# Kernel tuning notes

Hardware: AMD Instinct MI355X
Metric: run time of the kernel (lower is better)

Reference implementation:

```python
import jax, jax.numpy as jnp
import numpy as np

V = 10000   # vocab_size
L = 12      # n_layer
H = 12      # n_head
C = 768     # n_embd
TE = 64     # t_embd
WTE = C - TE
BS = 1024   # block_size
B, T = 4, 1024
D = C // H
EPS = 1e-5


def setup_inputs() -> dict:
    key = jax.random.key(0)
    ks = jax.random.split(key, 12)
    s = 0.02
    def n(k, shape, extra=1.0):
        return jax.random.normal(k, shape, jnp.float32) * (s * extra)
    resid_scale = 1.0 / np.sqrt(2 * L)  # c_proj init std scaling from _init_weights loop
    return {
        'idx': jax.random.randint(ks[0], (B, T), 0, V),
        'ts': jax.random.uniform(ks[1], (B, T), jnp.float32) * 100.0,
        'wte': n(ks[2], (V, WTE)),
        'basis_freq': jnp.asarray(1.0 / 10 ** np.linspace(0, 9, TE), jnp.float32),
        'phase': jnp.zeros((TE,), jnp.float32),
        'wpe': n(ks[3], (BS, C)),
        'ln1_w': jnp.ones((L, C), jnp.float32), 'ln1_b': jnp.zeros((L, C), jnp.float32),
        'qkv_w': n(ks[4], (L, 3 * C, C)), 'qkv_b': jnp.zeros((L, 3 * C), jnp.float32),
        'proj_w': n(ks[5], (L, C, C), resid_scale), 'proj_b': jnp.zeros((L, C), jnp.float32),
        'ln2_w': jnp.ones((L, C), jnp.float32), 'ln2_b': jnp.zeros((L, C), jnp.float32),
        'fc_w': n(ks[6], (L, 4 * C, C)), 'fc_b': jnp.zeros((L, 4 * C), jnp.float32),
        'fc2_w': n(ks[7], (L, C, 4 * C), resid_scale), 'fc2_b': jnp.zeros((L, C), jnp.float32),
        'lnf_w': jnp.ones((C,), jnp.float32), 'lnf_b': jnp.zeros((C,), jnp.float32),
        'lm_w': n(ks[8], (V, C)),
        'tp_w': n(ks[9], (1, C)),
    }


def _ln(x, w, b):
    mu = jnp.mean(x, -1, keepdims=True)
    var = jnp.mean((x - mu) ** 2, -1, keepdims=True)
    return (x - mu) * jax.lax.rsqrt(var + EPS) * w + b


def reference(idx, ts, wte, basis_freq, phase, wpe, ln1_w, ln1_b, qkv_w, qkv_b,
              proj_w, proj_b, ln2_w, ln2_b, fc_w, fc_b, fc2_w, fc2_b,
              lnf_w, lnf_b, lm_w, tp_w):
    Bv, Tv = idx.shape
    tok = wte[idx]                                      # [B,T,C-TE]
    tim = jnp.cos(ts[..., None] * basis_freq + phase)   # TimeEncode -> [B,T,TE]
    x = jnp.concatenate([tok, tim], axis=-1) + wpe[:Tv]
    mask = jnp.tril(jnp.ones((Tv, Tv), bool))
    scale = 1.0 / np.sqrt(D)

    def block(x, p):
        l1w, l1b, qw, qb, pw, pb, l2w, l2b, fw, fb, f2w, f2b = p
        h = _ln(x, l1w, l1b)
        qkv = h @ qw.T + qb                              # [B,T,3C]
        q, k, v = jnp.split(qkv, 3, axis=-1)
        def heads(z):
            return z.reshape(Bv, Tv, H, D).transpose(0, 2, 1, 3)  # [B,H,T,D]
        q, k, v = heads(q), heads(k), heads(v)
        att = jnp.einsum('bhtd,bhsd->bhts', q, k) * scale
        att = jnp.where(mask, att, -jnp.inf)             # causal masked_fill
        att = jax.nn.softmax(att, axis=-1)
        y = jnp.einsum('bhts,bhsd->bhtd', att, v)
        y = y.transpose(0, 2, 1, 3).reshape(Bv, Tv, C)
        x = x + (y @ pw.T + pb)
        h2 = _ln(x, l2w, l2b)
        m = jax.nn.gelu(h2 @ fw.T + fb, approximate=False)  # torch nn.GELU default is exact
        x = x + (m @ f2w.T + f2b)
        return x, None

    x, _ = jax.lax.scan(block, x, (ln1_w, ln1_b, qkv_w, qkv_b, proj_w, proj_b,
                                   ln2_w, ln2_b, fc_w, fc_b, fc2_w, fc2_b))
    x = _ln(x, lnf_w, lnf_b)
    logits = x @ lm_w.T          # [B,T,V]
    tpred = x @ tp_w.T           # [B,T,1]
    return logits, tpred
```

## Files before the change

### kernel.cpp

```cpp
#include <hip/hip_runtime.h>
#include <hip/hip_bf16.h>
#include <math.h>

#define Bb   4
#define Tt   1024
#define Cc   768
#define Hh   12
#define Dd   64
#define Ll   12
#define Vv   10000
#define WTEe 704
#define MTOT 4096

#define QSCALE 0.18033688f

typedef __bf16 bf16x8 __attribute__((ext_vector_type(8)));
typedef float  f32x4  __attribute__((ext_vector_type(4)));
typedef unsigned short u16;

typedef const __attribute__((address_space(1))) void* gptr_t;
typedef __attribute__((address_space(3))) void* lptr_t;

__device__ inline void gload16(const void* g, void* l) {
    __builtin_amdgcn_global_load_lds((gptr_t)g, (lptr_t)l, 16, 0, 0);
}

__device__ inline u16 f2bf(float f) {
    unsigned int u = __float_as_uint(f);
    return (u16)((u + 0x7fffu + ((u >> 16) & 1u)) >> 16);
}
__device__ inline float bf2f(u16 u) { return __uint_as_float(((unsigned)u) << 16); }

__device__ inline float gelu_f(float v) {
    float t = v * (0.797884561f + 0.0356774081f * v * v);
    float e = __expf(2.f * t);
    float th = 1.f - 2.f / (e + 1.f);
    return 0.5f * v * (1.f + th);
}

#if __has_builtin(__builtin_amdgcn_exp2f)
__device__ inline float fast_exp2(float x) { return __builtin_amdgcn_exp2f(x); }
#else
__device__ inline float fast_exp2(float x) { return exp2f(x); }
#endif

#define WAITVM(N)  asm volatile("s_waitcnt vmcnt(" #N ")" ::: "memory")
#define WAITLGKM0() asm volatile("s_waitcnt lgkmcnt(0)" ::: "memory")
#define SCHEDB()   __builtin_amdgcn_sched_barrier(0)
#define SBAR()     __builtin_amdgcn_s_barrier()

__global__ __launch_bounds__(256)
void convert_pack(const float* __restrict__ in, u16* __restrict__ out,
                  int nk8, int K, int rowmod, int scaleLim)
{
    int i = blockIdx.x * 256 + threadIdx.x;
    if (i >= nk8) return;
    int row = (i << 3) / K;
    int col = (i << 3) % K;
    float s = 1.f;
    if (rowmod && (row % rowmod) < scaleLim) s = QSCALE;
    float4 v0 = ((const float4*)in)[2 * i];
    float4 v1 = ((const float4*)in)[2 * i + 1];
    uint4 o;
    o.x = (unsigned)f2bf(v0.x * s) | ((unsigned)f2bf(v0.y * s) << 16);
    o.y = (unsigned)f2bf(v0.z * s) | ((unsigned)f2bf(v0.w * s) << 16);
    o.z = (unsigned)f2bf(v1.x * s) | ((unsigned)f2bf(v1.y * s) << 16);
    o.w = (unsigned)f2bf(v1.z * s) | ((unsigned)f2bf(v1.w * s) << 16);
    int tile = row >> 4, kt = col >> 5;
    int l = (row & 15) | (((col >> 3) & 3) << 4);
    size_t off = (((size_t)tile * (K >> 5) + kt) << 9) + l * 8;
    *(uint4*)(out + off) = o;
}

__global__ __launch_bounds__(256)
void scale_qkvb(const float* __restrict__ in, float* __restrict__ out, int n)
{
    int i = blockIdx.x * 256 + threadIdx.x;
    if (i >= n) return;
    int col = i % (3 * Cc);
    out[i] = in[i] * (col < Cc ? QSCALE : 1.f);
}

__global__ __launch_bounds__(256)
void embed_kernel(const int* __restrict__ idx, const float* __restrict__ ts,
                  const float* __restrict__ wte, const float* __restrict__ freq,
                  const float* __restrict__ ph, const float* __restrict__ wpe,
                  float* __restrict__ x)
{
    const int bt  = blockIdx.x;
    const int t   = bt & (Tt - 1);
    const int tok = idx[bt];
    const float tv = ts[bt];
#pragma unroll
    for (int j = 0; j < 3; ++j) {
        int c = threadIdx.x + (j << 8);
        float val;
        if (c < WTEe) val = wte[(size_t)tok * WTEe + c];
        else {
            int e = c - WTEe;
            val = cosf(tv * freq[e] + ph[e]);
        }
        x[(size_t)bt * Cc + c] = val + wpe[(size_t)t * Cc + c];
    }
}

__global__ __launch_bounds__(256)
void ln_kernel(const float* __restrict__ x, const float* __restrict__ wt,
               const float* __restrict__ bs, u16* __restrict__ out)
{
    const int row = blockIdx.x;
    const int tid = threadIdx.x;
    const float* xr = x + (size_t)row * Cc;
    float v0 = xr[tid], v1 = xr[tid + 256], v2 = xr[tid + 512];
    float s = v0 + v1 + v2;
#pragma unroll
    for (int m = 32; m; m >>= 1) s += __shfl_xor(s, m);
    __shared__ float red[4];
    const int wv = tid >> 6;
    if ((tid & 63) == 0) red[wv] = s;
    __syncthreads();
    float mu = (red[0] + red[1] + red[2] + red[3]) * (1.f / 768.f);
    float d0 = v0 - mu, d1 = v1 - mu, d2 = v2 - mu;
    float s2 = d0 * d0 + d1 * d1 + d2 * d2;
#pragma unroll
    for (int m = 32; m; m >>= 1) s2 += __shfl_xor(s2, m);
    __syncthreads();
    if ((tid & 63) == 0) red[wv] = s2;
    __syncthreads();
    float var = (red[0] + red[1] + red[2] + red[3]) * (1.f / 768.f);
    float rs = rsqrtf(var + 1e-5f);
    u16* orow = out + (size_t)row * Cc;
    orow[tid]       = f2bf(d0 * rs * wt[tid]       + bs[tid]);
    orow[tid + 256] = f2bf(d1 * rs * wt[tid + 256] + bs[tid + 256]);
    orow[tid + 512] = f2bf(d2 * rs * wt[tid + 512] + bs[tid + 512]);
}

__device__ inline void st_out(float* p, size_t o, float v) { p[o] = v; }
__device__ inline void st_out(u16*   p, size_t o, float v) { p[o] = f2bf(v); }

template<int EPI, typename OutT>
__global__ __launch_bounds__(256)
void gemm_bf16(const u16* __restrict__ A, const u16* __restrict__ Wp,
               const float* __restrict__ bias, const float* __restrict__ resid,
               OutT* __restrict__ out, u16* __restrict__ vt, int N, int K)
{
    __shared__ uint4 AF[3][8][64];
    __shared__ uint4 BF[3][8][64];
    const int tid  = threadIdx.x;
    const int lane = tid & 63;
    const int w    = tid >> 6;
    const int wr   = w >> 1, wc = w & 1;
    const int lq   = lane & 15, g = lane >> 4;
    const int m0   = blockIdx.x * 128, n0 = blockIdx.y * 128;
    const int KB   = K >> 5;

    const int arow0 = m0 + (2 * w) * 16 + lq;
    const int arow1 = arow0 + 16;
    const u16* ap0 = A + (size_t)arow0 * K + g * 8;
    const u16* ap1 = A + (size_t)arow1 * K + g * 8;

    int tn0 = (n0 >> 4) + 2 * w, tn1 = tn0 + 1;
    const int tmax = (N >> 4) - 1;
    tn0 = tn0 < tmax ? tn0 : tmax;
    tn1 = tn1 < tmax ? tn1 : tmax;
    const u16* bq0 = Wp + (((size_t)tn0 * KB) << 9) + lane * 8;
    const u16* bq1 = Wp + (((size_t)tn1 * KB) << 9) + lane * 8;

    f32x4 acc[4][4] = {};
    const int nk = KB;

#define GSTAGE(s, sl) do { int kk_ = (s) << 5;                      \
        gload16(ap0 + kk_, &AF[sl][2 * w][lane]);                   \
        gload16(ap1 + kk_, &AF[sl][2 * w + 1][lane]);               \
        gload16(bq0 + ((size_t)(s) << 9), &BF[sl][2 * w][lane]);    \
        gload16(bq1 + ((size_t)(s) << 9), &BF[sl][2 * w + 1][lane]); } while (0)

    GSTAGE(0, 0);
    GSTAGE(1, 1);
    WAITVM(4);
    SCHEDB();
    SBAR();
    SCHEDB();

    int sl = 0;
    for (int t = 0; t < nk; ++t) {
        int sl2 = sl + 2; if (sl2 >= 3) sl2 -= 3;
        if (t + 2 < nk) GSTAGE(t + 2, sl2);

        bf16x8 af[4], bfr[4];
#pragma unroll
        for (int mi = 0; mi < 4; ++mi)
            af[mi] = __builtin_bit_cast(bf16x8, AF[sl][wr * 4 + mi][lane]);
#pragma unroll
        for (int ni = 0; ni < 4; ++ni)
            bfr[ni] = __builtin_bit_cast(bf16x8, BF[sl][wc * 4 + ni][lane]);
        __builtin_amdgcn_s_setprio(1);
#pragma unroll
        for (int mi = 0; mi < 4; ++mi)
#pragma unroll
            for (int ni = 0; ni < 4; ++ni)
                acc[mi][ni] = __builtin_amdgcn_mfma_f32_16x16x32_bf16(
                    af[mi], bfr[ni], acc[mi][ni], 0, 0, 0);
        __builtin_amdgcn_s_setprio(0);

        if (t + 2 < nk) { WAITVM(4); }
        else           { WAITVM(0); }
        SCHEDB();
        SBAR();
        SCHEDB();
        sl = (sl + 1 == 3) ? 0 : sl + 1;
    }
#undef GSTAGE

    if (EPI == 3 && n0 >= 1536) {
#pragma unroll
        for (int mi = 0; mi < 4; ++mi)
#pragma unroll
            for (int ni = 0; ni < 4; ++ni) {
                int col = n0 + wc * 64 + ni * 16 + lq;
                int c2  = col - 1536;
                int hh  = c2 >> 6, dd = c2 & 63;
                int row = m0 + wr * 64 + mi * 16 + g * 4;
                int bb  = row >> 10, tr = row & 1023;
                float bv = bias[col];
                ushort4 o;
                o.x = f2bf(acc[mi][ni][0] + bv);
                o.y = f2bf(acc[mi][ni][1] + bv);
                o.z = f2bf(acc[mi][ni][2] + bv);
                o.w = f2bf(acc[mi][ni][3] + bv);
                *(ushort4*)&vt[(((size_t)bb * Hh + hh) * Dd + dd) * Tt + tr] = o;
            }
        return;
    }

#pragma unroll
    for (int mi = 0; mi < 4; ++mi)
#pragma unroll
        for (int ni = 0; ni < 4; ++ni) {
            int col = n0 + wc * 64 + ni * 16 + lq;
            if (col >= N) continue;
            int row = m0 + wr * 64 + mi * 16 + g * 4;
            float bv = bias ? bias[col] : 0.f;
#pragma unroll
            for (int q = 0; q < 4; ++q) {
                float v = acc[mi][ni][q] + bv;
                size_t o = (size_t)(row + q) * N + col;
                if (EPI == 1) v += resid[o];
                if (EPI == 2) v = gelu_f(v);
                st_out(out, o, v);
            }
        }
}

template<int EPI, typename OutT>
__global__ __launch_bounds__(256)
void gemm_n64(const u16* __restrict__ A, const u16* __restrict__ Wp,
              const float* __restrict__ bias, const float* __restrict__ resid,
              OutT* __restrict__ out, int N, int K)
{
    __shared__ uint4 AF[3][4][64];
    __shared__ uint4 BF[3][8][64];
    const int tid  = threadIdx.x;
    const int lane = tid & 63;
    const int w    = tid >> 6;
    const int wr   = w & 1, wc = w >> 1;
    const int lq   = lane & 15, g = lane >> 4;
    const int m0   = blockIdx.x * 64, n0 = blockIdx.y * 128;
    const int KB   = K >> 5;

    const u16* ap  = A + (size_t)(m0 + w * 16 + lq) * K + g * 8;
    int tn0 = (n0 >> 4) + 2 * w, tn1 = tn0 + 1;
    const int tmax = (N >> 4) - 1;
    tn0 = tn0 < tmax ? tn0 : tmax;
    tn1 = tn1 < tmax ? tn1 : tmax;
    const u16* bq0 = Wp + (((size_t)tn0 * KB) << 9) + lane * 8;
    const u16* bq1 = Wp + (((size_t)tn1 * KB) << 9) + lane * 8;

    f32x4 acc[2][4] = {};
    const int nk = KB;

#define GSTAGE(s, sl) do { int kk_ = (s) << 5;                      \
        gload16(ap  + kk_, &AF[sl][w][lane]);                       \
        gload16(bq0 + ((size_t)(s) << 9), &BF[sl][2 * w][lane]);    \
        gload16(bq1 + ((size_t)(s) << 9), &BF[sl][2 * w + 1][lane]); } while (0)

    GSTAGE(0, 0);
    GSTAGE(1, 1);
    WAITVM(3);
    SCHEDB();
    SBAR();
    SCHEDB();

    int sl = 0;
    for (int t = 0; t < nk; ++t) {
        int sl2 = sl + 2; if (sl2 >= 3) sl2 -= 3;
        if (t + 2 < nk) GSTAGE(t + 2, sl2);

        bf16x8 af[2], bfr[4];
#pragma unroll
        for (int mi = 0; mi < 2; ++mi)
            af[mi] = __builtin_bit_cast(bf16x8, AF[sl][wr * 2 + mi][lane]);
#pragma unroll
        for (int ni = 0; ni < 4; ++ni)
            bfr[ni] = __builtin_bit_cast(bf16x8, BF[sl][wc * 4 + ni][lane]);
        __builtin_amdgcn_s_setprio(1);
#pragma unroll
        for (int mi = 0; mi < 2; ++mi)
#pragma unroll
            for (int ni = 0; ni < 4; ++ni)
                acc[mi][ni] = __builtin_amdgcn_mfma_f32_16x16x32_bf16(
                    af[mi], bfr[ni], acc[mi][ni], 0, 0, 0);
        __builtin_amdgcn_s_setprio(0);

        if (t + 2 < nk) { WAITVM(3); }
        else           { WAITVM(0); }
        SCHEDB();
        SBAR();
        SCHEDB();
        sl = (sl + 1 == 3) ? 0 : sl + 1;
    }
#undef GSTAGE

#pragma unroll
    for (int mi = 0; mi < 2; ++mi)
#pragma unroll
        for (int ni = 0; ni < 4; ++ni) {
            int col = n0 + wc * 64 + ni * 16 + lq;
            if (col >= N) continue;
            int row = m0 + wr * 32 + mi * 16 + g * 4;
            float bv = bias ? bias[col] : 0.f;
#pragma unroll
            for (int q = 0; q < 4; ++q) {
                float v = acc[mi][ni][q] + bv;
                size_t o = (size_t)(row + q) * N + col;
                if (EPI == 1) v += resid[o];
                if (EPI == 2) v = gelu_f(v);
                st_out(out, o, v);
            }
        }
}

template<int EPI, typename OutT>
__global__ __launch_bounds__(512, 2)
void gemm8p(const u16* __restrict__ A, const u16* __restrict__ Wp,
            const float* __restrict__ bias, const float* __restrict__ resid,
            OutT* __restrict__ out, int N, int K)
{
    __shared__ uint4 AF[2][16][2][64];
    __shared__ uint4 BF[2][16][2][64];
    const int tid  = threadIdx.x;
    const int lane = tid & 63;
    const int w    = tid >> 6;
    const int wr   = w >> 2, wc = w & 3;
    const int lq   = lane & 15, g = lane >> 4;
    const int m0   = blockIdx.x * 256, n0 = blockIdx.y * 256;
    const int KB   = K >> 5;

    const int ar0 = m0 + (2 * w) * 16 + lq;
    const u16* aS0 = A + (size_t)ar0 * K + g * 8;
    const u16* aS1 = aS0 + (size_t)16 * K;

    int tn0 = (n0 >> 4) + 2 * w, tn1 = tn0 + 1;
    const int tmax = (N >> 4) - 1;
    tn0 = tn0 < tmax ? tn0 : tmax;
    tn1 = tn1 < tmax ? tn1 : tmax;
    const u16* bq0 = Wp + (((size_t)tn0 * KB) << 9) + lane * 8;
    const u16* bq1 = Wp + (((size_t)tn1 * KB) << 9) + lane * 8;

    f32x4 acc[8][4] = {};
    const int nt = K >> 6;

    gload16(aS0,      &AF[0][2 * w][0][lane]);
    gload16(aS1,      &AF[0][2 * w + 1][0][lane]);
    gload16(bq0,                 &BF[0][2 * w][0][lane]);
    gload16(bq1,                 &BF[0][2 * w + 1][0][lane]);
    gload16(aS0 + 32, &AF[0][2 * w][1][lane]);
    gload16(aS1 + 32, &AF[0][2 * w + 1][1][lane]);
    gload16(bq0 + 512,           &BF[0][2 * w][1][lane]);
    gload16(bq1 + 512,           &BF[0][2 * w + 1][1][lane]);
    WAITVM(0);
    SCHEDB();
    SBAR();

    int buf = 0;
    for (int t = 0; t < nt; ++t) {
        const bool more = (t + 1 < nt);
        const int kn = (t + 1) << 6;
        const size_t bb0 = (size_t)(2 * (t + 1)) << 9;
        bf16x8 a0[4], a1[4], b0[4];

#pragma unroll
        for (int i = 0; i < 4; ++i)
            a0[i] = __builtin_bit_cast(bf16x8, AF[buf][wr * 8 + i][0][lane]);
#pragma unroll
        for (int i = 0; i < 4; ++i)
            b0[i] = __builtin_bit_cast(bf16x8, BF[buf][wc * 4 + i][0][lane]);
        if (more) {
            gload16(aS0 + kn, &AF[buf ^ 1][2 * w][0][lane]);
            gload16(aS1 + kn, &AF[buf ^ 1][2 * w + 1][0][lane]);
        }
        SCHEDB();
        SBAR();
        WAITLGKM0();
        SCHEDB();
        __builtin_amdgcn_s_setprio(1);
#pragma unroll
        for (int mi = 0; mi < 4; ++mi)
#pragma unroll
            for (int ni = 0; ni < 4; ++ni)
                acc[mi][ni] = __builtin_amdgcn_mfma_f32_16x16x32_bf16(
                    a0[mi], b0[ni], acc[mi][ni], 0, 0, 0);
        __builtin_amdgcn_s_setprio(0);
        SBAR();

#pragma unroll
        for (int i = 0; i < 4; ++i)
            a1[i] = __builtin_bit_cast(bf16x8, AF[buf][wr * 8 + 4 + i][0][lane]);
        if (more) {
            gload16(bq0 + bb0, &BF[buf ^ 1][2 * w][0][lane]);
            gload16(bq1 + bb0, &BF[buf ^ 1][2 * w + 1][0][lane]);
        }
        SCHEDB();
        SBAR();
        WAITLGKM0();
        SCHEDB();
        __builtin_amdgcn_s_setprio(1);
#pragma unroll
        for (int mi = 0; mi < 4; ++mi)
#pragma unroll
            for (int ni = 0; ni < 4; ++ni)
                acc[4 + mi][ni] = __builtin_amdgcn_mfma_f32_16x16x32_bf16(
                    a1[mi], b0[ni], acc[4 + mi][ni], 0, 0, 0);
        __builtin_amdgcn_s_setprio(0);
        if (more) { WAITVM(4); } else { WAITVM(0); }
        SCHEDB();
        SBAR();

#pragma unroll
        for (int i = 0; i < 4; ++i)
            a0[i] = __builtin_bit_cast(bf16x8, AF[buf][wr * 8 + i][1][lane]);
#pragma unroll
        for (int i = 0; i < 4; ++i)
            b0[i] = __builtin_bit_cast(bf16x8, BF[buf][wc * 4 + i][1][lane]);
        if (more) {
            gload16(aS0 + kn + 32, &AF[buf ^ 1][2 * w][1][lane]);
            gload16(aS1 + kn + 32, &AF[buf ^ 1][2 * w + 1][1][lane]);
        }
        SCHEDB();
        SBAR();
        WAITLGKM0();
        SCHEDB();
        __builtin_amdgcn_s_setprio(1);
#pragma unroll
        for (int mi = 0; mi < 4; ++mi)
#pragma unroll
            for (int ni = 0; ni < 4; ++ni)
                acc[mi][ni] = __builtin_amdgcn_mfma_f32_16x16x32_bf16(
                    a0[mi], b0[ni], acc[mi][ni], 0, 0, 0);
        __builtin_amdgcn_s_setprio(0);
        SBAR();

#pragma unroll
        for (int i = 0; i < 4; ++i)
            a1[i] = __builtin_bit_cast(bf16x8, AF[buf][wr * 8 + 4 + i][1][lane]);
        if (more) {
            gload16(bq0 + bb0 + 512, &BF[buf ^ 1][2 * w][1][lane]);
            gload16(bq1 + bb0 + 512, &BF[buf ^ 1][2 * w + 1][1][lane]);
        }
        SCHEDB();
        SBAR();
        WAITLGKM0();
        SCHEDB();
        __builtin_amdgcn_s_setprio(1);
#pragma unroll
        for (int mi = 0; mi < 4; ++mi)
#pragma unroll
            for (int ni = 0; ni < 4; ++ni)
                acc[4 + mi][ni] = __builtin_amdgcn_mfma_f32_16x16x32_bf16(
                    a1[mi], b0[ni], acc[4 + mi][ni], 0, 0, 0);
        __builtin_amdgcn_s_setprio(0);
        if (more) { WAITVM(4); } else { WAITVM(0); }
        SCHEDB();
        SBAR();

        buf ^= 1;
    }

#pragma unroll
    for (int mi = 0; mi < 8; ++mi)
#pragma unroll
        for (int ni = 0; ni < 4; ++ni) {
            int col = n0 + wc * 64 + ni * 16 + lq;
            if (col >= N) continue;
            int row = m0 + wr * 128 + mi * 16 + g * 4;
            float bv = bias ? bias[col] : 0.f;
#pragma unroll
            for (int q = 0; q < 4; ++q) {
                float v = acc[mi][ni][q] + bv;
                size_t o = (size_t)(row + q) * N + col;
                if (EPI == 1) v += resid[o];
                if (EPI == 2) v = gelu_f(v);
                st_out(out, o, v);
            }
        }
}

__global__ __launch_bounds__(512)
void attn_mfma(const u16* __restrict__ qkv, const u16* __restrict__ vt,
               u16* __restrict__ y)
{
    __shared__ uint4 KF[2][4][2][64];
    __shared__ uint4 VF[2][4][2][64];

    const int tid  = threadIdx.x;
    const int lane = tid & 63;
    const int w    = tid >> 6;
    const int lq   = lane & 15, g = lane >> 4;
    const int m    = gridDim.x - 1 - blockIdx.x;
    const int bh   = blockIdx.y;
    const int b    = bh / Hh, h = bh % Hh;
    const int wq0  = m * 128 + w * 16;
    const size_t base = (size_t)b * Tt * (3 * Cc);

    const u16* qrow = qkv + base + (size_t)(wq0 + lq) * (3 * Cc) + h * Dd;
    bf16x8 qf0 = __builtin_bit_cast(bf16x8, *(const uint4*)(qrow + g * 8));
    bf16x8 qf1 = __builtin_bit_cast(bf16x8, *(const uint4*)(qrow + 32 + g * 8));

    f32x4 yac[4] = {};
    float lrun = 0.f;

    const int wm = w & 3;
    const u16* kbase = qkv + base + Cc + h * Dd + (size_t)(wm * 16 + lq) * (3 * Cc) + g * 8;
    const u16* vbase = vt + ((size_t)bh * Dd + wm * 16 + lq) * Tt + g * 8;

#define STAGE(c, bi)  do {                                              \
        if (w < 4) {                                                    \
            const u16* kp = kbase + (size_t)(c) * 64 * (3 * Cc);        \
            gload16(kp,      &KF[bi][wm][0][lane]);                     \
            gload16(kp + 32, &KF[bi][wm][1][lane]);                     \
        } else {                                                        \
            const u16* vp = vbase + (c) * 64;                           \
            gload16(vp,      &VF[bi][wm][0][lane]);                     \
            gload16(vp + 32, &VF[bi][wm][1][lane]);                     \
        }                                                               \
    } while (0)

    const int nch = 2 * m + 2;
    STAGE(0, 0);
    WAITVM(0);
    SCHEDB();
    SBAR();

    const int srcb = lq + ((g & 1) << 5);

    int buf = 0;
    for (int c = 0; c < nch; ++c) {
        if (c + 1 < nch) STAGE(c + 1, buf ^ 1);

        f32x4 sc[4] = {};
        __builtin_amdgcn_s_setprio(1);
#pragma unroll
        for (int nt = 0; nt < 4; ++nt) {
            bf16x8 k0 = __builtin_bit_cast(bf16x8, KF[buf][nt][0][lane]);
            bf16x8 k1 = __builtin_bit_cast(bf16x8, KF[buf][nt][1][lane]);
            sc[nt] = __builtin_amdgcn_mfma_f32_16x16x32_bf16(k0, qf0, sc[nt], 0, 0, 0);
            sc[nt] = __builtin_amdgcn_mfma_f32_16x16x32_bf16(k1, qf1, sc[nt], 0, 0, 0);
        }
        __builtin_amdgcn_s_setprio(0);

        const int s0 = c * 64;
        if (s0 + 63 > wq0) {
            const int qg = wq0 + lq;
#pragma unroll
            for (int nt = 0; nt < 4; ++nt) {
                const int kb = s0 + nt * 16 + (g << 2);
#pragma unroll
                for (int j = 0; j < 4; ++j)
                    if (kb + j > qg) sc[nt][j] = -1e30f;
            }
        }

        float ls = 0.f;
#pragma unroll
        for (int nt = 0; nt < 4; ++nt)
#pragma unroll
            for (int j = 0; j < 4; ++j) {
                float p = fast_exp2(sc[nt][j]);
                sc[nt][j] = p;
                ls += p;
            }
        ls += __shfl_xor(ls, 16);
        ls += __shfl_xor(ls, 32);
        lrun += ls;

        unsigned pk[4][2];
#pragma unroll
        for (int nt = 0; nt < 4; ++nt) {
            unsigned u0 = __float_as_uint(sc[nt][0]);
            unsigned u1 = __float_as_uint(sc[nt][1]);
            unsigned u2 = __float_as_uint(sc[nt][2]);
            unsigned u3 = __float_as_uint(sc[nt][3]);
            pk[nt][0] = (u0 >> 16) | (u1 & 0xffff0000u);
            pk[nt][1] = (u2 >> 16) | (u3 & 0xffff0000u);
        }

        unsigned pa0[4], pa1[4];
#pragma unroll
        for (int m2 = 0; m2 < 4; ++m2) {
            int hsel = m2 & 1;
            int src  = srcb + ((m2 >> 1) << 4);
            unsigned lo0 = __shfl(pk[0][hsel], src);
            unsigned hi0 = __shfl(pk[1][hsel], src);
            unsigned lo1 = __shfl(pk[2][hsel], src);
            unsigned hi1 = __shfl(pk[3][hsel], src);
            pa0[m2] = (g >> 1) ? hi0 : lo0;
            pa1[m2] = (g >> 1) ? hi1 : lo1;
        }
        uint4 A0 = make_uint4(pa0[0], pa0[1], pa0[2], pa0[3]);
        uint4 A1 = make_uint4(pa1[0], pa1[1], pa1[2], pa1[3]);
        bf16x8 pA0 = __builtin_bit_cast(bf16x8, A0);
        bf16x8 pA1 = __builtin_bit_cast(bf16x8, A1);

        __builtin_amdgcn_s_setprio(1);
#pragma unroll
        for (int dt = 0; dt < 4; ++dt) {
            bf16x8 vb0 = __builtin_bit_cast(bf16x8, VF[buf][dt][0][lane]);
            bf16x8 vb1 = __builtin_bit_cast(bf16x8, VF[buf][dt][1][lane]);
            yac[dt] = __builtin_amdgcn_mfma_f32_16x16x32_bf16(pA0, vb0, yac[dt], 0, 0, 0);
            yac[dt] = __builtin_amdgcn_mfma_f32_16x16x32_bf16(pA1, vb1, yac[dt], 0, 0, 0);
        }
        __builtin_amdgcn_s_setprio(0);

        if (c + 1 < nch) { WAITVM(0); }
        SCHEDB();
        SBAR();
        buf ^= 1;
    }
#undef STAGE

    f32x4 rl;
#pragma unroll
    for (int j = 0; j < 4; ++j)
        rl[j] = 1.0f / __shfl(lrun, (g << 2) + j);
#pragma unroll
    for (int dt = 0; dt < 4; ++dt)
#pragma unroll
        for (int j = 0; j < 4; ++j)
            y[(size_t)(b * Tt + wq0 + (g << 2) + j) * Cc + h * Dd + dt * 16 + lq]
                = f2bf(yac[dt][j] * rl[j]);
}

__global__ __launch_bounds__(256)
void tpred_kernel(const u16* __restrict__ h, const float* __restrict__ tp,
                  float* __restrict__ out)
{
    const int row  = blockIdx.x * 4 + (threadIdx.x >> 6);
    const int lane = threadIdx.x & 63;
    const u16* hr = h + (size_t)row * Cc;
    float s = 0.f;
#pragma unroll
    for (int j = 0; j < 12; ++j) s += bf2f(hr[lane + (j << 6)]) * tp[lane + (j << 6)];
#pragma unroll
    for (int m = 32; m; m >>= 1) s += __shfl_xor(s, m);
    if (lane == 0) out[row] = s;
}

extern "C" void kernel_launch(void* const* d_in, const int* in_sizes, int n_in,
                              void* d_out, int out_size, void* d_ws, size_t ws_size,
                              hipStream_t stream)
{
    const int*   idx  = (const int*)d_in[0];
    const float* ts   = (const float*)d_in[1];
    const float* wte  = (const float*)d_in[2];
    const float* freq = (const float*)d_in[3];
    const float* ph   = (const float*)d_in[4];
    const float* wpe  = (const float*)d_in[5];
    const float* ln1w = (const float*)d_in[6];
    const float* ln1b = (const float*)d_in[7];
    const float* qkvw = (const float*)d_in[8];
    const float* qkvb = (const float*)d_in[9];
    const float* pw   = (const float*)d_in[10];
    const float* pb   = (const float*)d_in[11];
    const float* ln2w = (const float*)d_in[12];
    const float* ln2b = (const float*)d_in[13];
    const float* fcw  = (const float*)d_in[14];
    const float* fcb  = (const float*)d_in[15];
    const float* f2w  = (const float*)d_in[16];
    const float* f2b  = (const float*)d_in[17];
    const float* lnfw = (const float*)d_in[18];
    const float* lnfb = (const float*)d_in[19];
    const float* lmw  = (const float*)d_in[20];
    const float* tpw  = (const float*)d_in[21];
    float* out = (float*)d_out;

    const int n_qkvw = 3 * Cc * Cc, n_pw = Cc * Cc, n_fcw = 4 * Cc * Cc;

    char* p = (char*)d_ws;
    float* x    = (float*)p;               p += (size_t)MTOT * Cc * 4;
    u16*   qkvB = (u16*)p;                 p += (size_t)MTOT * 3 * Cc * 2;
    u16*   VtB  = (u16*)p;                 p += (size_t)Bb * Hh * Dd * Tt * 2;
    u16*   hB   = (u16*)p;                 p += (size_t)MTOT * Cc * 2;
    u16*   yB   = (u16*)p;                 p += (size_t)MTOT * Cc * 2;
    u16*   mbB  = (u16*)p;                 p += (size_t)MTOT * 4 * Cc * 2;
    u16*   lmwB = (u16*)p;                 p += (size_t)Vv * Cc * 2;
    float* sbias= (float*)p;               p += (size_t)Ll * 3 * Cc * 4;
    char* wbase = p;

    size_t need_big = (size_t)(wbase - (char*)d_ws)
                    + ((size_t)Ll * (n_qkvw + n_pw + 2 * n_fcw)) * 2;
    bool big = ws_size >= need_big;

    u16 *wqA, *wpA, *wfA, *wf2A;
    if (big) {
        wqA  = (u16*)wbase;                wbase += (size_t)Ll * n_qkvw * 2;
        wpA  = (u16*)wbase;                wbase += (size_t)Ll * n_pw * 2;
        wfA  = (u16*)wbase;                wbase += (size_t)Ll * n_fcw * 2;
        wf2A = (u16*)wbase;
    } else {
        wqA  = (u16*)wbase;                wbase += (size_t)n_qkvw * 2;
        wpA  = (u16*)wbase;                wbase += (size_t)n_pw * 2;
        wfA  = (u16*)wbase;                wbase += (size_t)n_fcw * 2;
        wf2A = (u16*)wbase;
    }

    auto pack = [&](const float* src, u16* dst, size_t rows, int K,
                    int rowmod, int scaleLim) {
        int nk8 = (int)(rows * K / 8);
        convert_pack<<<(nk8 + 255) / 256, 256, 0, stream>>>(
            src, dst, nk8, K, rowmod, scaleLim);
    };

    pack(lmw, lmwB, Vv, Cc, 0, 0);
    {
        int nb = Ll * 3 * Cc;
        scale_qkvb<<<(nb + 255) / 256, 256, 0, stream>>>(qkvb, sbias, nb);
    }
    if (big) {
        pack(qkvw, wqA,  (size_t)Ll * 3 * Cc, Cc, 3 * Cc, Cc);
        pack(pw,   wpA,  (size_t)Ll * Cc,     Cc, 0, 0);
        pack(fcw,  wfA,  (size_t)Ll * 4 * Cc, Cc, 0, 0);
        pack(f2w,  wf2A, (size_t)Ll * Cc, 4 * Cc, 0, 0);
    }
    embed_kernel<<<MTOT, 256, 0, stream>>>(idx, ts, wte, freq, ph, wpe, x);

    for (int l = 0; l < Ll; ++l) {
        u16 *wqB, *wpB, *wfB, *wf2B;
        if (big) {
            wqB  = wqA  + (size_t)l * n_qkvw;
            wpB  = wpA  + (size_t)l * n_pw;
            wfB  = wfA  + (size_t)l * n_fcw;
            wf2B = wf2A + (size_t)l * n_fcw;
        } else {
            wqB = wqA; wpB = wpA; wfB = wfA; wf2B = wf2A;
            pack(qkvw + (size_t)l * n_qkvw, wqB, 3 * Cc, Cc, 3 * Cc, Cc);
            pack(pw   + (size_t)l * n_pw,   wpB, Cc,     Cc, 0, 0);
            pack(fcw  + (size_t)l * n_fcw,  wfB, 4 * Cc, Cc, 0, 0);
            pack(f2w  + (size_t)l * n_fcw,  wf2B, Cc, 4 * Cc, 0, 0);
        }

        ln_kernel<<<MTOT, 256, 0, stream>>>(x, ln1w + l * Cc, ln1b + l * Cc, hB);
        gemm_bf16<3, u16><<<dim3(32, 18), 256, 0, stream>>>(
            hB, wqB, sbias + (size_t)l * 3 * Cc, nullptr, qkvB, VtB, 3 * Cc, Cc);
        attn_mfma<<<dim3(Tt / 128, Bb * Hh), 512, 0, stream>>>(qkvB, VtB, yB);
        gemm_n64<1, float><<<dim3(64, 6), 256, 0, stream>>>(
            yB, wpB, pb + (size_t)l * Cc, x, x, Cc, Cc);
        ln_kernel<<<MTOT, 256, 0, stream>>>(x, ln2w + l * Cc, ln2b + l * Cc, hB);
        gemm_bf16<2, u16><<<dim3(32, 24), 256, 0, stream>>>(
            hB, wfB, fcb + (size_t)l * 4 * Cc, nullptr, mbB, nullptr, 4 * Cc, Cc);
        gemm_n64<1, float><<<dim3(64, 6), 256, 0, stream>>>(
            mbB, wf2B, f2b + (size_t)l * Cc, x, x, Cc, 4 * Cc);
    }

    ln_kernel<<<MTOT, 256, 0, stream>>>(x, lnfw, lnfb, hB);
    gemm8p<0, float><<<dim3(16, 40), 512, 0, stream>>>(
        hB, lmwB, nullptr, nullptr, out, Vv, Cc);
    tpred_kernel<<<MTOT / 4, 256, 0, stream>>>(hB, tpw, out + (size_t)MTOT * Vv);
}
```

Measured before the change: 2.764 ms.

## Load attention K/V directly to registers and swizzle LM-head GEMM block order

The attention kernel drops its LDS double buffer and barriers. Each wave now loads its K and V fragments straight from global memory into registers, prefetching the next K chunk. Blocks shrink to 4 waves covering 64 queries, so the grid doubles to 16 tiles per head. Separately, the LM-head GEMM uses a 1D grid with an XCD-aware swizzle to improve L2 locality across chiplets. The trade-off is redundant global K/V loads per wave and higher register pressure.

Result: slower. 3.440 ms (+24.4%).

```diff
diff --git a/kernel.cpp b/kernel.cpp
--- a/kernel.cpp
+++ b/kernel.cpp
@@ -344,7 +344,7 @@
 __global__ __launch_bounds__(512, 2)
 void gemm8p(const u16* __restrict__ A, const u16* __restrict__ Wp,
             const float* __restrict__ bias, const float* __restrict__ resid,
-            OutT* __restrict__ out, int N, int K)
+            OutT* __restrict__ out, int N, int K, int MB)
 {
     __shared__ uint4 AF[2][16][2][64];
     __shared__ uint4 BF[2][16][2][64];
@@ -353,7 +353,10 @@
     const int w    = tid >> 6;
     const int wr   = w >> 2, wc = w & 3;
     const int lq   = lane & 15, g = lane >> 4;
-    const int m0   = blockIdx.x * 256, n0 = blockIdx.y * 256;
+    const int bid  = blockIdx.x;
+    const int cpx  = gridDim.x >> 3;
+    const int swz  = (bid & 7) * cpx + (bid >> 3);
+    const int m0   = (swz % MB) * 256, n0 = (swz / MB) * 256;
     const int KB   = K >> 5;
 
     const int ar0 = m0 + (2 * w) * 16 + lq;
@@ -505,13 +508,10 @@
         }
 }
 
-__global__ __launch_bounds__(512)
+__global__ __launch_bounds__(256)
 void attn_mfma(const u16* __restrict__ qkv, const u16* __restrict__ vt,
                u16* __restrict__ y)
 {
-    __shared__ uint4 KF[2][4][2][64];
-    __shared__ uint4 VF[2][4][2][64];
-
     const int tid  = threadIdx.x;
     const int lane = tid & 63;
     const int w    = tid >> 6;
@@ -519,7 +519,7 @@
     const int m    = gridDim.x - 1 - blockIdx.x;
     const int bh   = blockIdx.y;
     const int b    = bh / Hh, h = bh % Hh;
-    const int wq0  = m * 128 + w * 16;
+    const int wq0  = m * 64 + w * 16;
     const size_t base = (size_t)b * Tt * (3 * Cc);
 
     const u16* qrow = qkv + base + (size_t)(wq0 + lq) * (3 * Cc) + h * Dd;
@@ -529,40 +529,42 @@
     f32x4 yac[4] = {};
     float lrun = 0.f;
 
-    const int wm = w & 3;
-    const u16* kbase = qkv + base + Cc + h * Dd + (size_t)(wm * 16 + lq) * (3 * Cc) + g * 8;
-    const u16* vbase = vt + ((size_t)bh * Dd + wm * 16 + lq) * Tt + g * 8;
-
-#define STAGE(c, bi)  do {                                              \
-        if (w < 4) {                                                    \
-            const u16* kp = kbase + (size_t)(c) * 64 * (3 * Cc);        \
-            gload16(kp,      &KF[bi][wm][0][lane]);                     \
-            gload16(kp + 32, &KF[bi][wm][1][lane]);                     \
-        } else {                                                        \
-            const u16* vp = vbase + (c) * 64;                           \
-            gload16(vp,      &VF[bi][wm][0][lane]);                     \
-            gload16(vp + 32, &VF[bi][wm][1][lane]);                     \
-        }                                                               \
+    const u16* kroot = qkv + base + Cc + (size_t)lq * (3 * Cc) + h * Dd + g * 8;
+    const u16* vroot = vt + ((size_t)bh * Dd + lq) * Tt + g * 8;
+
+#define LDK(arr, c) do {                                                     \
+        _Pragma("unroll")                                                    \
+        for (int nt_ = 0; nt_ < 4; ++nt_)                                    \
+            _Pragma("unroll")                                                \
+            for (int s_ = 0; s_ < 2; ++s_)                                   \
+                arr[nt_][s_] = *(const uint4*)(kroot                         \
+                    + (size_t)((c) * 64 + nt_ * 16) * (3 * Cc) + s_ * 32);   \
     } while (0)
-
-    const int nch = 2 * m + 2;
-    STAGE(0, 0);
-    WAITVM(0);
-    SCHEDB();
-    SBAR();
-
+#define LDV(arr, c) do {                                                     \
+        _Pragma("unroll")                                                    \
+        for (int dt_ = 0; dt_ < 4; ++dt_)                                    \
+            _Pragma("unroll")                                                \
+            for (int s_ = 0; s_ < 2; ++s_)                                   \
+                arr[dt_][s_] = *(const uint4*)(vroot                         \
+                    + (size_t)(dt_ * 16) * Tt + (c) * 64 + s_ * 32);         \
+    } while (0)
+
+    const int nch = m + 1;
     const int srcb = lq + ((g & 1) << 5);
 
-    int buf = 0;
+    uint4 kc[4][2], kn[4][2], vc[4][2];
+    LDK(kc, 0);
+
     for (int c = 0; c < nch; ++c) {
-        if (c + 1 < nch) STAGE(c + 1, buf ^ 1);
+        LDV(vc, c);
+        if (c + 1 < nch) LDK(kn, c + 1);
 
         f32x4 sc[4] = {};
         __builtin_amdgcn_s_setprio(1);
 #pragma unroll
         for (int nt = 0; nt < 4; ++nt) {
-            bf16x8 k0 = __builtin_bit_cast(bf16x8, KF[buf][nt][0][lane]);
-            bf16x8 k1 = __builtin_bit_cast(bf16x8, KF[buf][nt][1][lane]);
+            bf16x8 k0 = __builtin_bit_cast(bf16x8, kc[nt][0]);
+            bf16x8 k1 = __builtin_bit_cast(bf16x8, kc[nt][1]);
             sc[nt] = __builtin_amdgcn_mfma_f32_16x16x32_bf16(k0, qf0, sc[nt], 0, 0, 0);
             sc[nt] = __builtin_amdgcn_mfma_f32_16x16x32_bf16(k1, qf1, sc[nt], 0, 0, 0);
         }
@@ -624,19 +626,23 @@
         __builtin_amdgcn_s_setprio(1);
 #pragma unroll
         for (int dt = 0; dt < 4; ++dt) {
-            bf16x8 vb0 = __builtin_bit_cast(bf16x8, VF[buf][dt][0][lane]);
-            bf16x8 vb1 = __builtin_bit_cast(bf16x8, VF[buf][dt][1][lane]);
+            bf16x8 vb0 = __builtin_bit_cast(bf16x8, vc[dt][0]);
+            bf16x8 vb1 = __builtin_bit_cast(bf16x8, vc[dt][1]);
             yac[dt] = __builtin_amdgcn_mfma_f32_16x16x32_bf16(pA0, vb0, yac[dt], 0, 0, 0);
             yac[dt] = __builtin_amdgcn_mfma_f32_16x16x32_bf16(pA1, vb1, yac[dt], 0, 0, 0);
         }
         __builtin_amdgcn_s_setprio(0);
 
-        if (c + 1 < nch) { WAITVM(0); }
-        SCHEDB();
-        SBAR();
-        buf ^= 1;
-    }
-#undef STAGE
+        if (c + 1 < nch) {
+#pragma unroll
+            for (int nt = 0; nt < 4; ++nt)
+#pragma unroll
+                for (int s = 0; s < 2; ++s)
+                    kc[nt][s] = kn[nt][s];
+        }
+    }
+#undef LDK
+#undef LDV
 
     f32x4 rl;
 #pragma unroll
@@ -761,7 +767,7 @@
         ln_kernel<<<MTOT, 256, 0, stream>>>(x, ln1w + l * Cc, ln1b + l * Cc, hB);
         gemm_bf16<3, u16><<<dim3(32, 18), 256, 0, stream>>>(
             hB, wqB, sbias + (size_t)l * 3 * Cc, nullptr, qkvB, VtB, 3 * Cc, Cc);
-        attn_mfma<<<dim3(Tt / 128, Bb * Hh), 512, 0, stream>>>(qkvB, VtB, yB);
+        attn_mfma<<<dim3(16, Bb * Hh), 256, 0, stream>>>(qkvB, VtB, yB);
         gemm_n64<1, float><<<dim3(64, 6), 256, 0, stream>>>(
             yB, wpB, pb + (size_t)l * Cc, x, x, Cc, Cc);
         ln_kernel<<<MTOT, 256, 0, stream>>>(x, ln2w + l * Cc, ln2b + l * Cc, hB);
@@ -772,7 +778,7 @@
     }
 
     ln_kernel<<<MTOT, 256, 0, stream>>>(x, lnfw, lnfb, hB);
-    gemm8p<0, float><<<dim3(16, 40), 512, 0, stream>>>(
-        hB, lmwB, nullptr, nullptr, out, Vv, Cc);
+    gemm8p<0, float><<<640, 512, 0, stream>>>(
+        hB, lmwB, nullptr, nullptr, out, Vv, Cc, 16);
     tpred_kernel<<<MTOT / 4, 256, 0, stream>>>(hB, tpw, out + (size_t)MTOT * Vv);
 }
```
